# Optimization experiments

Measured on AMD Instinct MI355X. Metric: run time of the kernel, lower is better.

Reference implementation:

```python
import jax, jax.numpy as jnp
import numpy as np

N_NODES = 50000
N_EDGES = 800000
EDGE_F = 96
NODE_F = 256
GLOB_F = 64
HIDDEN = 1024
N_GRAPHS = 8
MLP_IN = NODE_F + 3 * EDGE_F + GLOB_F  # 608


def setup_inputs() -> dict:
    key = jax.random.key(0)
    ks = jax.random.split(key, 9)
    x = jax.random.normal(ks[0], (N_NODES, NODE_F), dtype=jnp.float32)
    edge_attr = jax.random.normal(ks[1], (N_EDGES, EDGE_F), dtype=jnp.float32)
    u = jax.random.normal(ks[2], (N_GRAPHS, GLOB_F), dtype=jnp.float32)
    W1 = jax.random.normal(ks[3], (MLP_IN, HIDDEN), dtype=jnp.float32) * (1.0 / np.sqrt(MLP_IN))
    b1 = jax.random.normal(ks[4], (HIDDEN,), dtype=jnp.float32) * 0.01
    W2 = jax.random.normal(ks[5], (HIDDEN, NODE_F), dtype=jnp.float32) * (1.0 / np.sqrt(HIDDEN))
    b2 = jax.random.normal(ks[6], (NODE_F,), dtype=jnp.float32) * 0.01
    edge_index = jax.random.randint(ks[7], (2, N_EDGES), 0, N_NODES, dtype=jnp.int64 if jax.config.jax_enable_x64 else jnp.int32)
    batch = jnp.sort(jax.random.randint(ks[8], (N_NODES,), 0, N_GRAPHS, dtype=jnp.int32))
    return {"x": x, "edge_attr": edge_attr, "u": u, "W1": W1, "b1": b1,
            "W2": W2, "b2": b2, "edge_index": edge_index, "batch": batch}


def reference(x, edge_attr, u, W1, b1, W2, b2, edge_index, batch):
    col = edge_index[1]  # destination node for each edge
    n = x.shape[0]
    # sum / max / mean segment reductions over edges -> per-node features
    out1 = jax.ops.segment_sum(edge_attr, col, num_segments=n)                     # [N, E_F]
    cnt = jax.ops.segment_sum(jnp.ones((edge_attr.shape[0], 1), edge_attr.dtype), col, num_segments=n)  # [N,1]
    out2 = jax.ops.segment_max(edge_attr, col, num_segments=n)
    out2 = jnp.where(cnt > 0, out2, jnp.zeros_like(out2))  # torch_scatter gives 0 for empty segments
    out3 = out1 / jnp.maximum(cnt, 1.0)                    # mean; 0 for empty segments
    h = jnp.concatenate([x, out1, out2, out3, u[batch]], axis=1)  # [N, 608]
    h = jax.nn.relu(h @ W1 + b1) @ W2 + b2                        # node MLP
    return h + x  # residual
```

## Files before the change

### kernel.cpp

```cpp
#include <hip/hip_runtime.h>
#include <stdint.h>

#define N_NODES 50000
#define N_EDGES 800000
#define EDGE_F  96
#define NODE_F  256
#define GLOB_F  64
#define HIDDEN  1024
#define MLP_IN  608
#define M_PAD   50048
#define SCAN_BLOCKS 196

typedef __bf16 bf16;
typedef __bf16 bf16x8 __attribute__((ext_vector_type(8)));
typedef float  f32x4  __attribute__((ext_vector_type(4)));

typedef __attribute__((address_space(1))) unsigned int gu32;
typedef __attribute__((address_space(3))) unsigned int lu32;

__device__ __forceinline__ void glds16(const void* g, void* l) {
    __builtin_amdgcn_global_load_lds((const gu32*)g, (lu32*)l, 16, 0, 0);
}

static constexpr size_t H_OFF    = 0;
static constexpr size_t H_BYTES  = (size_t)M_PAD * MLP_IN * 2;
static constexpr size_t HID_OFF  = H_OFF + H_BYTES;
static constexpr size_t HID_BYTES= (size_t)M_PAD * HIDDEN * 2;
static constexpr size_t W1T_OFF  = HID_OFF + HID_BYTES;
static constexpr size_t W1T_BYTES= (size_t)HIDDEN * MLP_IN * 2;
static constexpr size_t W2T_OFF  = W1T_OFF + W1T_BYTES;
static constexpr size_t W2T_BYTES= (size_t)NODE_F * HIDDEN * 2;
static constexpr size_t DEG_OFF  = W2T_OFF + W2T_BYTES;
static constexpr size_t DEG_BYTES= 200192;
static constexpr size_t CUR_OFF  = DEG_OFF + DEG_BYTES;
static constexpr size_t CUR_BYTES= 200192;
static constexpr size_t START_OFF= CUR_OFF + CUR_BYTES;
static constexpr size_t START_BYTES = 200192;
static constexpr size_t EIDS_OFF = START_OFF + START_BYTES;
static constexpr size_t EIDS_BYTES = (size_t)N_EDGES * 4;
static constexpr size_t BSUM_OFF = EIDS_OFF + EIDS_BYTES;
static constexpr size_t BSUM_BYTES = 1024;
static constexpr size_t BOFF_OFF = BSUM_OFF + BSUM_BYTES;

__global__ __launch_bounds__(256) void hist_kernel(const int* __restrict__ col,
                                                   int* __restrict__ deg) {
    int e = blockIdx.x * 256 + threadIdx.x;
    if (e < N_EDGES) atomicAdd(&deg[col[e]], 1);
}

__global__ __launch_bounds__(256) void scan_phase1(const int* __restrict__ deg,
                                                   int* __restrict__ start,
                                                   int* __restrict__ bsum) {
    __shared__ int sc[256];
    const int t = threadIdx.x, b = blockIdx.x;
    const int idx = b * 256 + t;
    int v = (idx < N_NODES) ? deg[idx] : 0;
    sc[t] = v;
    __syncthreads();
    for (int off = 1; off < 256; off <<= 1) {
        int add = (t >= off) ? sc[t - off] : 0;
        __syncthreads();
        sc[t] += add;
        __syncthreads();
    }
    if (idx < N_NODES) start[idx] = sc[t] - v;
    if (t == 255) bsum[b] = sc[255];
}

__global__ __launch_bounds__(256) void scan_phase2(int* __restrict__ bsum,
                                                   int* __restrict__ boff,
                                                   int* __restrict__ start) {
    __shared__ int sc[256];
    const int t = threadIdx.x;
    int v = (t < SCAN_BLOCKS) ? bsum[t] : 0;
    sc[t] = v;
    __syncthreads();
    for (int off = 1; off < 256; off <<= 1) {
        int add = (t >= off) ? sc[t - off] : 0;
        __syncthreads();
        sc[t] += add;
        __syncthreads();
    }
    if (t < SCAN_BLOCKS) boff[t] = sc[t] - v;
    if (t == 255) start[N_NODES] = sc[255];
}

__global__ __launch_bounds__(256) void scan_phase3(int* __restrict__ start,
                                                   const int* __restrict__ boff) {
    const int idx = blockIdx.x * 256 + threadIdx.x;
    if (idx < N_NODES) start[idx] += boff[blockIdx.x];
}

__global__ __launch_bounds__(256) void scatter_kernel(const int* __restrict__ col,
                                                      const int* __restrict__ start,
                                                      int* __restrict__ cursor,
                                                      int* __restrict__ eids) {
    int e = blockIdx.x * 256 + threadIdx.x;
    if (e < N_EDGES) {
        int c = col[e];
        int p = start[c] + atomicAdd(&cursor[c], 1);
        eids[p] = e;
    }
}

#define BH_CHUNK 128
__global__ __launch_bounds__(128) void build_h_kernel(const float* __restrict__ x,
                                                      const float* __restrict__ edge_attr,
                                                      const float* __restrict__ u,
                                                      const int* __restrict__ batch,
                                                      const int* __restrict__ start,
                                                      const int* __restrict__ eids,
                                                      bf16* __restrict__ H) {
    const int n = blockIdx.x;
    const int t = threadIdx.x;
    bf16* row = H + (size_t)n * MLP_IN;
    if (n >= N_NODES) {
        for (int c = t; c < MLP_IN; c += 128) row[c] = (bf16)0.0f;
        return;
    }
    if (t < 64) {
        float4 v = ((const float4*)(x + (size_t)n * NODE_F))[t];
        row[t * 4 + 0] = (bf16)v.x;
        row[t * 4 + 1] = (bf16)v.y;
        row[t * 4 + 2] = (bf16)v.z;
        row[t * 4 + 3] = (bf16)v.w;
    } else {
        int g = batch[n];
        row[544 + (t - 64)] = (bf16)u[g * GLOB_F + (t - 64)];
    }

    __shared__ int se[BH_CHUNK];
    const int s0 = start[n], s1 = start[n + 1];
    float sm = 0.0f, mx = -3.0e38f;
    for (int base = s0; base < s1; base += BH_CHUNK) {
        const int cnt = min(BH_CHUNK, s1 - base);
        __syncthreads();
        if (t < cnt) se[t] = eids[base + t];
        __syncthreads();
        if (t < EDGE_F) {
            int i = 0;
            for (; i + 8 <= cnt; i += 8) {
                float v0 = edge_attr[(size_t)se[i + 0] * EDGE_F + t];
                float v1 = edge_attr[(size_t)se[i + 1] * EDGE_F + t];
                float v2 = edge_attr[(size_t)se[i + 2] * EDGE_F + t];
                float v3 = edge_attr[(size_t)se[i + 3] * EDGE_F + t];
                float v4 = edge_attr[(size_t)se[i + 4] * EDGE_F + t];
                float v5 = edge_attr[(size_t)se[i + 5] * EDGE_F + t];
                float v6 = edge_attr[(size_t)se[i + 6] * EDGE_F + t];
                float v7 = edge_attr[(size_t)se[i + 7] * EDGE_F + t];
                sm += ((v0 + v1) + (v2 + v3)) + ((v4 + v5) + (v6 + v7));
                float m01 = fmaxf(v0, v1), m23 = fmaxf(v2, v3);
                float m45 = fmaxf(v4, v5), m67 = fmaxf(v6, v7);
                mx = fmaxf(mx, fmaxf(fmaxf(m01, m23), fmaxf(m45, m67)));
            }
            for (; i + 2 <= cnt; i += 2) {
                float v0 = edge_attr[(size_t)se[i + 0] * EDGE_F + t];
                float v1 = edge_attr[(size_t)se[i + 1] * EDGE_F + t];
                sm += v0 + v1;
                mx = fmaxf(mx, fmaxf(v0, v1));
            }
            if (i < cnt) {
                float v = edge_attr[(size_t)se[i] * EDGE_F + t];
                sm += v;
                mx = fmaxf(mx, v);
            }
        }
    }
    if (t < EDGE_F) {
        int d = s1 - s0;
        if (d == 0) mx = 0.0f;
        float mean = sm / fmaxf((float)d, 1.0f);
        row[256 + t] = (bf16)sm;
        row[352 + t] = (bf16)mx;
        row[448 + t] = (bf16)mean;
    }
}

__global__ __launch_bounds__(256) void transpose_kernel(const float* __restrict__ W,
                                                        bf16* __restrict__ Wt,
                                                        int K, int N) {
    __shared__ float tile[32][33];
    const int tx = threadIdx.x & 31, ty = threadIdx.x >> 5;
    const int n0 = blockIdx.x * 32, k0 = blockIdx.y * 32;
#pragma unroll
    for (int r = 0; r < 4; r++)
        tile[ty + 8 * r][tx] = W[(size_t)(k0 + ty + 8 * r) * N + (n0 + tx)];
    __syncthreads();
#pragma unroll
    for (int r = 0; r < 4; r++)
        Wt[(size_t)(n0 + ty + 8 * r) * K + (k0 + tx)] = (bf16)tile[tx][ty + 8 * r];
}

__global__ __launch_bounds__(256) void gemm1_kernel(const bf16* __restrict__ H,
                                                    const bf16* __restrict__ Wt,
                                                    const float* __restrict__ b1,
                                                    bf16* __restrict__ hid) {
    __shared__ __align__(16) bf16 As[128 * 32];
    __shared__ __align__(16) bf16 Bs[128 * 32];
    const int t = threadIdx.x;
    const int wave = t >> 6, lane = t & 63;
    const int quad = lane >> 4, l16 = lane & 15;
    const int wm = (wave & 1) << 6, wn = (wave >> 1) << 6;
    const int bm = blockIdx.x, bn = blockIdx.y;

    f32x4 acc[4][4] = {};

    const char* Ag = (const char*)H  + (size_t)bm * 128 * (MLP_IN * 2);
    const char* Bg = (const char*)Wt + (size_t)bn * 128 * (MLP_IN * 2);
    const int srow = t >> 2, scc = t & 3;
    const size_t rowoff = (size_t)srow * (MLP_IN * 2) + scc * 16;
    char* Al = (char*)As + t * 16;
    char* Bl = (char*)Bs + t * 16;

    for (int k0 = 0; k0 < MLP_IN; k0 += 32) {
        __syncthreads();
        const char* a0 = Ag + rowoff + k0 * 2;
        glds16(a0, Al);
        glds16(a0 + (size_t)64 * (MLP_IN * 2), Al + 4096);
        const char* b0 = Bg + rowoff + k0 * 2;
        glds16(b0, Bl);
        glds16(b0 + (size_t)64 * (MLP_IN * 2), Bl + 4096);
        __syncthreads();
        bf16x8 a[4], b[4];
#pragma unroll
        for (int i = 0; i < 4; i++) a[i] = *(const bf16x8*)&As[(wm + i * 16 + l16) * 32 + quad * 8];
#pragma unroll
        for (int i = 0; i < 4; i++) b[i] = *(const bf16x8*)&Bs[(wn + i * 16 + l16) * 32 + quad * 8];
#pragma unroll
        for (int i = 0; i < 4; i++)
#pragma unroll
            for (int j = 0; j < 4; j++)
                acc[i][j] = __builtin_amdgcn_mfma_f32_16x16x32_bf16(a[i], b[j], acc[i][j], 0, 0, 0);
    }
#pragma unroll
    for (int i = 0; i < 4; i++) {
        int row0 = bm * 128 + wm + i * 16 + quad * 4;
#pragma unroll
        for (int j = 0; j < 4; j++) {
            int col = bn * 128 + wn + j * 16 + l16;
            float bias = b1[col];
#pragma unroll
            for (int r = 0; r < 4; r++) {
                float v = acc[i][j][r] + bias;
                v = fmaxf(v, 0.0f);
                hid[(size_t)(row0 + r) * HIDDEN + col] = (bf16)v;
            }
        }
    }
}

__global__ __launch_bounds__(256) void gemm2_kernel(const bf16* __restrict__ Hd,
                                                    const bf16* __restrict__ Wt,
                                                    const float* __restrict__ b2,
                                                    const float* __restrict__ x,
                                                    float* __restrict__ out) {
    __shared__ __align__(16) bf16 As[128 * 32];
    __shared__ __align__(16) bf16 Bs[128 * 32];
    const int t = threadIdx.x;
    const int wave = t >> 6, lane = t & 63;
    const int quad = lane >> 4, l16 = lane & 15;
    const int wm = (wave & 1) << 6, wn = (wave >> 1) << 6;
    const int bm = blockIdx.x, bn = blockIdx.y;

    f32x4 acc[4][4] = {};

    const char* Ag = (const char*)Hd + (size_t)bm * 128 * (HIDDEN * 2);
    const char* Bg = (const char*)Wt + (size_t)bn * 128 * (HIDDEN * 2);
    const int srow = t >> 2, scc = t & 3;
    const size_t rowoff = (size_t)srow * (HIDDEN * 2) + scc * 16;
    char* Al = (char*)As + t * 16;
    char* Bl = (char*)Bs + t * 16;

    for (int k0 = 0; k0 < HIDDEN; k0 += 32) {
        __syncthreads();
        const char* a0 = Ag + rowoff + k0 * 2;
        glds16(a0, Al);
        glds16(a0 + (size_t)64 * (HIDDEN * 2), Al + 4096);
        const char* b0 = Bg + rowoff + k0 * 2;
        glds16(b0, Bl);
        glds16(b0 + (size_t)64 * (HIDDEN * 2), Bl + 4096);
        __syncthreads();
        bf16x8 a[4], b[4];
#pragma unroll
        for (int i = 0; i < 4; i++) a[i] = *(const bf16x8*)&As[(wm + i * 16 + l16) * 32 + quad * 8];
#pragma unroll
        for (int i = 0; i < 4; i++) b[i] = *(const bf16x8*)&Bs[(wn + i * 16 + l16) * 32 + quad * 8];
#pragma unroll
        for (int i = 0; i < 4; i++)
#pragma unroll
            for (int j = 0; j < 4; j++)
                acc[i][j] = __builtin_amdgcn_mfma_f32_16x16x32_bf16(a[i], b[j], acc[i][j], 0, 0, 0);
    }
#pragma unroll
    for (int i = 0; i < 4; i++) {
        int row0 = bm * 128 + wm + i * 16 + quad * 4;
#pragma unroll
        for (int j = 0; j < 4; j++) {
            int col = bn * 128 + wn + j * 16 + l16;
            float bias = b2[col];
#pragma unroll
            for (int r = 0; r < 4; r++) {
                int row = row0 + r;
                if (row < N_NODES) {
                    size_t idx = (size_t)row * NODE_F + col;
                    out[idx] = acc[i][j][r] + bias + x[idx];
                }
            }
        }
    }
}

extern "C" void kernel_launch(void* const* d_in, const int* in_sizes, int n_in,
                              void* d_out, int out_size, void* d_ws, size_t ws_size,
                              hipStream_t stream) {
    const float* x         = (const float*)d_in[0];
    const float* edge_attr = (const float*)d_in[1];
    const float* u         = (const float*)d_in[2];
    const float* W1        = (const float*)d_in[3];
    const float* b1        = (const float*)d_in[4];
    const float* W2        = (const float*)d_in[5];
    const float* b2        = (const float*)d_in[6];
    const int*   edge_index= (const int*)d_in[7];
    const int*   batch     = (const int*)d_in[8];
    float*       out       = (float*)d_out;

    char* ws = (char*)d_ws;
    bf16* H    = (bf16*)(ws + H_OFF);
    bf16* hid  = (bf16*)(ws + HID_OFF);
    bf16* W1t  = (bf16*)(ws + W1T_OFF);
    bf16* W2t  = (bf16*)(ws + W2T_OFF);
    int*  deg  = (int*)(ws + DEG_OFF);
    int*  cur  = (int*)(ws + CUR_OFF);
    int*  start= (int*)(ws + START_OFF);
    int*  eids = (int*)(ws + EIDS_OFF);
    int*  bsum = (int*)(ws + BSUM_OFF);
    int*  boff = (int*)(ws + BOFF_OFF);

    const int* col = edge_index + N_EDGES;

    hipMemsetAsync(ws + DEG_OFF, 0, DEG_BYTES + CUR_BYTES, stream);
    hist_kernel<<<(N_EDGES + 255) / 256, 256, 0, stream>>>(col, deg);
    scan_phase1<<<SCAN_BLOCKS, 256, 0, stream>>>(deg, start, bsum);
    scan_phase2<<<1, 256, 0, stream>>>(bsum, boff, start);
    scan_phase3<<<SCAN_BLOCKS, 256, 0, stream>>>(start, boff);
    scatter_kernel<<<(N_EDGES + 255) / 256, 256, 0, stream>>>(col, start, cur, eids);
    build_h_kernel<<<M_PAD, 128, 0, stream>>>(x, edge_attr, u, batch, start, eids, H);
    transpose_kernel<<<dim3(HIDDEN / 32, MLP_IN / 32), 256, 0, stream>>>(W1, W1t, MLP_IN, HIDDEN);
    transpose_kernel<<<dim3(NODE_F / 32, HIDDEN / 32), 256, 0, stream>>>(W2, W2t, HIDDEN, NODE_F);
    gemm1_kernel<<<dim3(M_PAD / 128, HIDDEN / 128), 256, 0, stream>>>(H, W1t, b1, hid);
    gemm2_kernel<<<dim3(M_PAD / 128, NODE_F / 128), 256, 0, stream>>>(hid, W2t, b2, x, out);
}
```

Baseline: 798.2 us.

## Rewrite gemm1 as 256x256 double-buffered swizzled LDS pipeline with padded K

Result: faster. 769.9 us (-3.6%).

```diff
diff --git a/kernel.cpp b/kernel.cpp
--- a/kernel.cpp
+++ b/kernel.cpp
@@ -8,8 +8,10 @@
 #define GLOB_F  64
 #define HIDDEN  1024
 #define MLP_IN  608
-#define M_PAD   50048
+#define KP      640
+#define M_PAD   50176
 #define SCAN_BLOCKS 196
+#define NT1     10
 
 typedef __bf16 bf16;
 typedef __bf16 bf16x8 __attribute__((ext_vector_type(8)));
@@ -23,11 +25,11 @@
 }
 
 static constexpr size_t H_OFF    = 0;
-static constexpr size_t H_BYTES  = (size_t)M_PAD * MLP_IN * 2;
+static constexpr size_t H_BYTES  = (size_t)M_PAD * KP * 2;
 static constexpr size_t HID_OFF  = H_OFF + H_BYTES;
 static constexpr size_t HID_BYTES= (size_t)M_PAD * HIDDEN * 2;
 static constexpr size_t W1T_OFF  = HID_OFF + HID_BYTES;
-static constexpr size_t W1T_BYTES= (size_t)HIDDEN * MLP_IN * 2;
+static constexpr size_t W1T_BYTES= (size_t)HIDDEN * KP * 2;
 static constexpr size_t W2T_OFF  = W1T_OFF + W1T_BYTES;
 static constexpr size_t W2T_BYTES= (size_t)NODE_F * HIDDEN * 2;
 static constexpr size_t DEG_OFF  = W2T_OFF + W2T_BYTES;
@@ -113,9 +115,9 @@
                                                       bf16* __restrict__ H) {
     const int n = blockIdx.x;
     const int t = threadIdx.x;
-    bf16* row = H + (size_t)n * MLP_IN;
+    bf16* row = H + (size_t)n * KP;
     if (n >= N_NODES) {
-        for (int c = t; c < MLP_IN; c += 128) row[c] = (bf16)0.0f;
+        for (int c = t; c < KP; c += 128) row[c] = (bf16)0.0f;
         return;
     }
     if (t < 64) {
@@ -128,6 +130,7 @@
         int g = batch[n];
         row[544 + (t - 64)] = (bf16)u[g * GLOB_F + (t - 64)];
     }
+    if (t >= 96) row[608 + (t - 96)] = (bf16)0.0f;
 
     __shared__ int se[BH_CHUNK];
     const int s0 = start[n], s1 = start[n + 1];
@@ -178,75 +181,148 @@
 
 __global__ __launch_bounds__(256) void transpose_kernel(const float* __restrict__ W,
                                                         bf16* __restrict__ Wt,
-                                                        int K, int N) {
+                                                        int K, int N, int Kpad) {
     __shared__ float tile[32][33];
     const int tx = threadIdx.x & 31, ty = threadIdx.x >> 5;
     const int n0 = blockIdx.x * 32, k0 = blockIdx.y * 32;
+    if (k0 < K) {
+#pragma unroll
+        for (int r = 0; r < 4; r++)
+            tile[ty + 8 * r][tx] = W[(size_t)(k0 + ty + 8 * r) * N + (n0 + tx)];
+    }
+    __syncthreads();
 #pragma unroll
     for (int r = 0; r < 4; r++)
-        tile[ty + 8 * r][tx] = W[(size_t)(k0 + ty + 8 * r) * N + (n0 + tx)];
-    __syncthreads();
-#pragma unroll
-    for (int r = 0; r < 4; r++)
-        Wt[(size_t)(n0 + ty + 8 * r) * K + (k0 + tx)] = (bf16)tile[tx][ty + 8 * r];
-}
-
-__global__ __launch_bounds__(256) void gemm1_kernel(const bf16* __restrict__ H,
+        Wt[(size_t)(n0 + ty + 8 * r) * Kpad + (k0 + tx)] =
+            (k0 < K) ? (bf16)tile[tx][ty + 8 * r] : (bf16)0.0f;
+}
+
+#define VMC(n) asm volatile("s_waitcnt vmcnt(" #n ")" ::: "memory")
+#define LGK0   asm volatile("s_waitcnt lgkmcnt(0)" ::: "memory")
+#define BARR   __builtin_amdgcn_s_barrier()
+
+__global__ __launch_bounds__(512) void gemm1_kernel(const bf16* __restrict__ H,
                                                     const bf16* __restrict__ Wt,
                                                     const float* __restrict__ b1,
                                                     bf16* __restrict__ hid) {
-    __shared__ __align__(16) bf16 As[128 * 32];
-    __shared__ __align__(16) bf16 Bs[128 * 32];
+    __shared__ __align__(16) bf16 As[2][256 * 64];
+    __shared__ __align__(16) bf16 Bs[2][256 * 64];
     const int t = threadIdx.x;
     const int wave = t >> 6, lane = t & 63;
     const int quad = lane >> 4, l16 = lane & 15;
-    const int wm = (wave & 1) << 6, wn = (wave >> 1) << 6;
-    const int bm = blockIdx.x, bn = blockIdx.y;
-
-    f32x4 acc[4][4] = {};
-
-    const char* Ag = (const char*)H  + (size_t)bm * 128 * (MLP_IN * 2);
-    const char* Bg = (const char*)Wt + (size_t)bn * 128 * (MLP_IN * 2);
-    const int srow = t >> 2, scc = t & 3;
-    const size_t rowoff = (size_t)srow * (MLP_IN * 2) + scc * 16;
-    char* Al = (char*)As + t * 16;
-    char* Bl = (char*)Bs + t * 16;
-
-    for (int k0 = 0; k0 < MLP_IN; k0 += 32) {
-        __syncthreads();
-        const char* a0 = Ag + rowoff + k0 * 2;
-        glds16(a0, Al);
-        glds16(a0 + (size_t)64 * (MLP_IN * 2), Al + 4096);
-        const char* b0 = Bg + rowoff + k0 * 2;
-        glds16(b0, Bl);
-        glds16(b0 + (size_t)64 * (MLP_IN * 2), Bl + 4096);
-        __syncthreads();
-        bf16x8 a[4], b[4];
-#pragma unroll
-        for (int i = 0; i < 4; i++) a[i] = *(const bf16x8*)&As[(wm + i * 16 + l16) * 32 + quad * 8];
-#pragma unroll
-        for (int i = 0; i < 4; i++) b[i] = *(const bf16x8*)&Bs[(wn + i * 16 + l16) * 32 + quad * 8];
-#pragma unroll
-        for (int i = 0; i < 4; i++)
-#pragma unroll
-            for (int j = 0; j < 4; j++)
-                acc[i][j] = __builtin_amdgcn_mfma_f32_16x16x32_bf16(a[i], b[j], acc[i][j], 0, 0, 0);
-    }
-#pragma unroll
-    for (int i = 0; i < 4; i++) {
-        int row0 = bm * 128 + wm + i * 16 + quad * 4;
-#pragma unroll
-        for (int j = 0; j < 4; j++) {
-            int col = bn * 128 + wn + j * 16 + l16;
-            float bias = b1[col];
-#pragma unroll
-            for (int r = 0; r < 4; r++) {
-                float v = acc[i][j][r] + bias;
+    const int wr = wave >> 2;
+    const int wc = wave & 3;
+    const int bn = blockIdx.x, bm = blockIdx.y;
+
+    f32x4 acc[8][4] = {};
+    bf16x8 a[4][2], b[2][2];
+
+    const int srow = t >> 3;
+    const int scb  = (((t & 7) ^ (srow & 7)) << 4);
+    const char* Ag = (const char*)H  + (size_t)(bm * 256) * (KP * 2);
+    const char* Bg = (const char*)Wt + (size_t)(bn * 256) * (KP * 2);
+    char* AsB = (char*)&As[0][0];
+    char* BsB = (char*)&Bs[0][0];
+
+    const int swzl = (l16 & 7) << 4;
+    const int col0 = (quad * 16) ^ swzl;
+    const int col1 = (64 + quad * 16) ^ swzl;
+
+#define STG_A(buf, h, kt) do { \
+    const char* _s = Ag + (size_t)((h) * 128) * (KP * 2) + (size_t)(kt) * 128; \
+    char* _d = AsB + (buf) * 32768 + (h) * 16384 + t * 16; \
+    glds16(_s + (size_t)srow * (KP * 2) + scb, _d); \
+    glds16(_s + (size_t)(srow + 64) * (KP * 2) + scb, _d + 8192); \
+} while (0)
+#define STG_B(buf, h, kt) do { \
+    const char* _s = Bg + (size_t)((h) * 128) * (KP * 2) + (size_t)(kt) * 128; \
+    char* _d = BsB + (buf) * 32768 + (h) * 16384 + t * 16; \
+    glds16(_s + (size_t)srow * (KP * 2) + scb, _d); \
+    glds16(_s + (size_t)(srow + 64) * (KP * 2) + scb, _d + 8192); \
+} while (0)
+#define LDA(cbase, mq) do { \
+    _Pragma("unroll") for (int i = 0; i < 4; ++i) { \
+        const char* _p = (cbase) + (size_t)((mq) * 128 + wr * 64 + i * 16 + l16) * 128; \
+        a[i][0] = *(const bf16x8*)(_p + col0); \
+        a[i][1] = *(const bf16x8*)(_p + col1); \
+    } } while (0)
+#define LDB(cbase, nq) do { \
+    _Pragma("unroll") for (int j = 0; j < 2; ++j) { \
+        const char* _p = (cbase) + (size_t)((nq) * 128 + wc * 32 + j * 16 + l16) * 128; \
+        b[j][0] = *(const bf16x8*)(_p + col0); \
+        b[j][1] = *(const bf16x8*)(_p + col1); \
+    } } while (0)
+#define MMAQ(mq, nq) do { \
+    __builtin_amdgcn_s_setprio(1); \
+    _Pragma("unroll") for (int i = 0; i < 4; ++i) \
+    _Pragma("unroll") for (int j = 0; j < 2; ++j) { \
+        acc[(mq)*4+i][(nq)*2+j] = __builtin_amdgcn_mfma_f32_16x16x32_bf16(a[i][0], b[j][0], acc[(mq)*4+i][(nq)*2+j], 0, 0, 0); \
+        acc[(mq)*4+i][(nq)*2+j] = __builtin_amdgcn_mfma_f32_16x16x32_bf16(a[i][1], b[j][1], acc[(mq)*4+i][(nq)*2+j], 0, 0, 0); \
+    } \
+    __builtin_amdgcn_s_setprio(0); \
+} while (0)
+
+    STG_A(0, 0, 0);
+    STG_B(0, 0, 0);
+    STG_B(0, 1, 0);
+    STG_A(0, 1, 0);
+    VMC(4);
+    BARR;
+
+#pragma unroll 1
+    for (int kt = 0; kt < NT1 - 1; ++kt) {
+        const int c = kt & 1, o = c ^ 1;
+        const char* Ac = AsB + c * 32768;
+        const char* Bc = BsB + c * 32768;
+        LDA(Ac, 0); LDB(Bc, 0);
+        STG_A(o, 0, kt + 1);
+        VMC(4); BARR; LGK0;
+        MMAQ(0, 0); BARR;
+        LDB(Bc, 1);
+        STG_B(o, 0, kt + 1);
+        VMC(4); BARR; LGK0;
+        MMAQ(0, 1); BARR;
+        LDA(Ac, 1);
+        STG_B(o, 1, kt + 1);
+        BARR; LGK0;
+        MMAQ(1, 1); BARR;
+        LDB(Bc, 0);
+        STG_A(o, 1, kt + 1);
+        VMC(4); BARR; LGK0;
+        MMAQ(1, 0); BARR;
+    }
+    {
+        const int c = (NT1 - 1) & 1;
+        const char* Ac = AsB + c * 32768;
+        const char* Bc = BsB + c * 32768;
+        LDA(Ac, 0); LDB(Bc, 0); VMC(2); BARR; LGK0; MMAQ(0, 0); BARR;
+        LDB(Bc, 1);             VMC(0); BARR; LGK0; MMAQ(0, 1); BARR;
+        LDA(Ac, 1);                     BARR; LGK0; MMAQ(1, 1); BARR;
+        LDB(Bc, 0);                           LGK0; MMAQ(1, 0);
+    }
+
+#pragma unroll
+    for (int m = 0; m < 8; ++m) {
+        const int mq = m >> 2, i = m & 3;
+        const int row0 = bm * 256 + mq * 128 + wr * 64 + i * 16 + quad * 4;
+#pragma unroll
+        for (int n = 0; n < 4; ++n) {
+            const int nq = n >> 1, j = n & 1;
+            const int col = bn * 256 + nq * 128 + wc * 32 + j * 16 + l16;
+            const float bias = b1[col];
+#pragma unroll
+            for (int r = 0; r < 4; ++r) {
+                float v = acc[m][n][r] + bias;
                 v = fmaxf(v, 0.0f);
                 hid[(size_t)(row0 + r) * HIDDEN + col] = (bf16)v;
             }
         }
     }
+#undef STG_A
+#undef STG_B
+#undef LDA
+#undef LDB
+#undef MMAQ
 }
 
 __global__ __launch_bounds__(256) void gemm2_kernel(const bf16* __restrict__ Hd,
@@ -345,8 +421,8 @@
     scan_phase3<<<SCAN_BLOCKS, 256, 0, stream>>>(start, boff);
     scatter_kernel<<<(N_EDGES + 255) / 256, 256, 0, stream>>>(col, start, cur, eids);
     build_h_kernel<<<M_PAD, 128, 0, stream>>>(x, edge_attr, u, batch, start, eids, H);
-    transpose_kernel<<<dim3(HIDDEN / 32, MLP_IN / 32), 256, 0, stream>>>(W1, W1t, MLP_IN, HIDDEN);
-    transpose_kernel<<<dim3(NODE_F / 32, HIDDEN / 32), 256, 0, stream>>>(W2, W2t, HIDDEN, NODE_F);
-    gemm1_kernel<<<dim3(M_PAD / 128, HIDDEN / 128), 256, 0, stream>>>(H, W1t, b1, hid);
-    gemm2_kernel<<<dim3(M_PAD / 128, NODE_F / 128), 256, 0, stream>>>(hid, W2t, b2, x, out);
-}
+    transpose_kernel<<<dim3(HIDDEN / 32, KP / 32), 256, 0, stream>>>(W1, W1t, MLP_IN, HIDDEN, KP);
+    transpose_kernel<<<dim3(NODE_F / 32, HIDDEN / 32), 256, 0, stream>>>(W2, W2t, HIDDEN, NODE_F, HIDDEN);
+    gemm1_kernel<<<dim3(HIDDEN / 256, M_PAD / 256), 512, 0, stream>>>(H, W1t, b1, hid);
+    gemm2_kernel<<<dim3(391, 2), 256, 0, stream>>>(hid, W2t, b2, x, out);
+}
```
